# Performance work log

Hardware: AMD Instinct MI355X
Metric: run time of the kernel (lower is better)

The kernel has to match this reference:

```python
import jax, jax.numpy as jnp
import numpy as np

ALPHA = 16
M_FACTORS = [8, 16, 8]
N_FACTORS = [8, 16, 8]


def setup_inputs() -> dict:
    key = jax.random.key(0)
    ks = jax.random.split(key, 9)
    B, S, D = 8, 2048, 1024
    r = 8
    x = jax.random.normal(ks[0], (B, S, D), dtype=jnp.float32)
    W = jax.random.normal(ks[1], (D, D), dtype=jnp.float32) * 0.02
    b = jax.random.normal(ks[2], (D,), dtype=jnp.float32) * 0.02
    # m-cores: (r_prev, m_i, r_next), first rank = 1
    core0 = jax.random.normal(ks[3], (1, 8, r), dtype=jnp.float32) * 0.1
    core1 = jax.random.normal(ks[4], (r, 16, r), dtype=jnp.float32) * 0.1
    core2 = jax.random.normal(ks[5], (r, 8, r), dtype=jnp.float32) * 0.1
    # n-cores: (r_prev, n_i, r_next), last rank = 1
    core3 = jax.random.normal(ks[6], (r, 8, r), dtype=jnp.float32) * 0.1
    core4 = jax.random.normal(ks[7], (r, 16, r), dtype=jnp.float32) * 0.1
    core5 = jax.random.normal(ks[8], (r, 8, 1), dtype=jnp.float32) * 0.1
    return {"x": x, "W": W, "b": b, "core0": core0, "core1": core1,
            "core2": core2, "core3": core3, "core4": core4, "core5": core5}


def tensorized_multiplication(x, m_cores, n_cores, m_factors):
    B, S, _ = x.shape
    # [B, 1, S, m_k, ..., m_1] : input dim split into m_factors, reversed
    tt = x.reshape((B, S) + tuple(m_factors[::-1]))[:, None]
    for core in m_cores:
        # contract trailing m-factor and current rank, new rank at axis 1
        tt = jnp.einsum('br...m,rmp->bp...', tt, core)
    for core in n_cores:
        # expand n-factor at the end, carry rank at axis 1
        tt = jnp.einsum('br...,rnp->bp...n', tt, core)
    # tt: [B, 1, S, n_1, ..., n_k] -> [B, S, prod(n_factors)]
    return tt.reshape(B, S, -1)


def reference(x, W, b, core0, core1, core2, core3, core4, core5):
    z = tensorized_multiplication(x, [core0, core1, core2],
                                  [core3, core4, core5], M_FACTORS)
    base = jnp.einsum('bsd,od->bso', x, W) + b  # nn.Linear: x @ W.T + b
    return base + z * ALPHA
```

## Files before the change

### kernel.cpp

```cpp
#include <hip/hip_runtime.h>
#include <hip/hip_bf16.h>


#define D_DIM 1024
#define BS_ROWS 16384
#define ALPHA_F 16.0f
#define BM 128
#define BN 128

using bf16   = __bf16;
using bf16x8 = __attribute__((ext_vector_type(8))) __bf16;
using bf16x4 = __attribute__((ext_vector_type(4))) __bf16;
using f32x4  = __attribute__((ext_vector_type(4))) float;

#define GPTR(p) (const __attribute__((address_space(1))) void*)(p)
#define SPTR(p) (__attribute__((address_space(3))) void*)(p)

__global__ __launch_bounds__(256) void prep_kernel(
    const float* __restrict__ X,
    const float* __restrict__ W,
    const float* __restrict__ c0, const float* __restrict__ c1,
    const float* __restrict__ c2, const float* __restrict__ c3,
    const float* __restrict__ c4, const float* __restrict__ c5,
    bf16* __restrict__ Weff, bf16* __restrict__ Xb)
{
    __shared__ float t2[1024];
    __shared__ float Msh[8192];
    const int tid = threadIdx.x;

    if (blockIdx.x >= 1024) {
        size_t i = ((size_t)(blockIdx.x - 1024) * 256 + tid) * 8;
        f32x4 a = *(const f32x4*)&X[i];
        f32x4 b = *(const f32x4*)&X[i + 4];
        bf16x8 v;
        v[0] = (bf16)a[0]; v[1] = (bf16)a[1]; v[2] = (bf16)a[2]; v[3] = (bf16)a[3];
        v[4] = (bf16)b[0]; v[5] = (bf16)b[1]; v[6] = (bf16)b[2]; v[7] = (bf16)b[3];
        *(bf16x8*)&Xb[i] = v;
        return;
    }

    const int o = blockIdx.x;
    for (int e = tid; e < 1024; e += 256) {
        int p2 = e & 7, i2i1 = e >> 3;
        int i1 = i2i1 & 7, i2 = i2i1 >> 3;
        float s = 0.f;
        for (int p1 = 0; p1 < 8; ++p1)
            s += c0[i1 * 8 + p1] * c1[p1 * 128 + i2 * 8 + p2];
        t2[e] = s;
    }
    __syncthreads();
    for (int e = tid; e < 8192; e += 256) {
        int p3 = e & 7, d = e >> 3;
        int i1 = d & 7, i2 = (d >> 3) & 15, i3 = d >> 7;
        float s = 0.f;
        for (int p2 = 0; p2 < 8; ++p2)
            s += t2[(i2 * 8 + i1) * 8 + p2] * c2[p2 * 64 + i3 * 8 + p3];
        Msh[e] = s;
    }

    int n1 = o >> 7, nn = o & 127, n2 = nn >> 3, n3 = nn & 7;
    float v[8];
    for (int p4 = 0; p4 < 8; ++p4) {
        float s = 0.f;
        for (int p5 = 0; p5 < 8; ++p5)
            s += c4[p4 * 128 + n2 * 8 + p5] * c5[p5 * 8 + n3];
        v[p4] = s;
    }
    float ncol[8];
    for (int r3 = 0; r3 < 8; ++r3) {
        float s = 0.f;
        for (int p4 = 0; p4 < 8; ++p4)
            s += c3[r3 * 64 + n1 * 8 + p4] * v[p4];
        ncol[r3] = s;
    }
    __syncthreads();

    int d0 = tid * 4;
    f32x4 w = *(const f32x4*)&W[o * D_DIM + d0];
    bf16x4 res;
    for (int k = 0; k < 4; ++k) {
        float acc = 0.f;
        for (int r = 0; r < 8; ++r)
            acc += Msh[(d0 + k) * 8 + r] * ncol[r];
        res[k] = (bf16)(w[k] + ALPHA_F * acc);
    }
    *(bf16x4*)&Weff[o * D_DIM + d0] = res;
}

#define TBM 256
#define TBN 128
#define ABYTES (TBM * 128)
#define BBYTES (TBN * 128)
#define BUFB   (ABYTES + BBYTES)
#define NBUFS  3
#define NTILES (D_DIM / 64)

__global__ __launch_bounds__(512, 2) void gemm_pipe_kernel(
    const bf16* __restrict__ Xb,
    const bf16* __restrict__ Weff,
    const float* __restrict__ bias,
    float* __restrict__ Out)
{
    extern __shared__ __attribute__((aligned(16))) char smem[];

    const int tid  = threadIdx.x;
    const int wave = tid >> 6, lane = tid & 63;

    const int bid   = blockIdx.x;
    const int slot  = (bid & 7) * 64 + (bid >> 3);
    const int mtile = slot >> 3;
    const int ntile = slot & 7;

    const int wr = wave >> 1, wc = wave & 1;
    const int l15 = lane & 15, quad = lane >> 4;
    const int rsw = l15 & 7;

    const int srow   = wave * 8 + (lane >> 3);
    const int gchunk = (lane & 7) ^ (lane >> 3);
    const bf16* asrc = Xb   + (size_t)(mtile * TBM + srow) * D_DIM + gchunk * 8;
    const bf16* bsrc = Weff + (size_t)(ntile * TBN + srow) * D_DIM + gchunk * 8;
    const int woff = wave * 1024;

    auto STAGE = [&](int bo, int t) {
        const bf16* ap = asrc + t * 64;
        const bf16* bp = bsrc + t * 64;
        char* ad = smem + bo + woff;
        char* bd = smem + bo + ABYTES + woff;
#pragma unroll
        for (int j = 0; j < 4; ++j)
            __builtin_amdgcn_global_load_lds(GPTR(ap + (size_t)j * 64 * D_DIM),
                                             SPTR(ad + j * 8192), 16, 0, 0);
#pragma unroll
        for (int j = 0; j < 2; ++j)
            __builtin_amdgcn_global_load_lds(GPTR(bp + (size_t)j * 64 * D_DIM),
                                             SPTR(bd + j * 8192), 16, 0, 0);
    };

    f32x4 acc[4][4];
#pragma unroll
    for (int i = 0; i < 4; ++i)
#pragma unroll
        for (int j = 0; j < 4; ++j)
#pragma unroll
            for (int r = 0; r < 4; ++r) acc[i][j][r] = 0.f;

    auto COMPUTE = [&](int bo) {
        const bf16* Ab = (const bf16*)(smem + bo);
        const bf16* Bb = (const bf16*)(smem + bo + ABYTES);
#pragma unroll
        for (int kk = 0; kk < 2; ++kk) {
            const int sc = ((kk * 4 + quad) ^ rsw) * 8;
            bf16x8 af[4], bfr[4];
#pragma unroll
            for (int i = 0; i < 4; ++i)
                af[i] = *(const bf16x8*)&Ab[(wr * 64 + i * 16 + l15) * 64 + sc];
#pragma unroll
            for (int j = 0; j < 4; ++j)
                bfr[j] = *(const bf16x8*)&Bb[(wc * 64 + j * 16 + l15) * 64 + sc];
            __builtin_amdgcn_s_setprio(1);
#pragma unroll
            for (int i = 0; i < 4; ++i)
#pragma unroll
                for (int j = 0; j < 4; ++j)
                    acc[i][j] = __builtin_amdgcn_mfma_f32_16x16x32_bf16(
                        af[i], bfr[j], acc[i][j], 0, 0, 0);
            __builtin_amdgcn_s_setprio(0);
        }
    };

    STAGE(0, 0);
    STAGE(BUFB, 1);
    asm volatile("s_waitcnt vmcnt(6)" ::: "memory");
    __builtin_amdgcn_s_barrier();
    __builtin_amdgcn_sched_barrier(0);

    int bo = 0;
#pragma unroll
    for (int t = 0; t < NTILES - 2; ++t) {
        int bs = bo + 2 * BUFB; if (bs >= NBUFS * BUFB) bs -= NBUFS * BUFB;
        STAGE(bs, t + 2);
        COMPUTE(bo);
        asm volatile("s_waitcnt vmcnt(6) lgkmcnt(0)" ::: "memory");
        __builtin_amdgcn_s_barrier();
        __builtin_amdgcn_sched_barrier(0);
        bo += BUFB; if (bo == NBUFS * BUFB) bo = 0;
    }
    COMPUTE(bo);
    asm volatile("s_waitcnt vmcnt(0) lgkmcnt(0)" ::: "memory");
    __builtin_amdgcn_s_barrier();
    __builtin_amdgcn_sched_barrier(0);
    bo += BUFB; if (bo == NBUFS * BUFB) bo = 0;
    COMPUTE(bo);

    float bj[4];
#pragma unroll
    for (int j = 0; j < 4; ++j)
        bj[j] = bias[ntile * TBN + wc * 64 + j * 16 + l15];
#pragma unroll
    for (int i = 0; i < 4; ++i) {
        int row0 = mtile * TBM + wr * 64 + i * 16 + quad * 4;
#pragma unroll
        for (int r = 0; r < 4; ++r) {
            float* orow = Out + (size_t)(row0 + r) * D_DIM + ntile * TBN + wc * 64 + l15;
#pragma unroll
            for (int j = 0; j < 4; ++j)
                orow[j * 16] = acc[i][j][r] + bj[j];
        }
    }
}

__global__ __launch_bounds__(256) void gemm_bb_kernel(
    const bf16* __restrict__ Xb,
    const bf16* __restrict__ Weff,
    const float* __restrict__ bias,
    float* __restrict__ Out)
{
    __shared__ __align__(16) bf16 As[BM][64];
    __shared__ __align__(16) bf16 Bs[BN][64];

    const int tid  = threadIdx.x;
    const int wave = tid >> 6, lane = tid & 63;
    const int mtile = blockIdx.x, ntile = blockIdx.y;
    const int wr = wave >> 1, wc = wave & 1;
    const int l15 = lane & 15, quad = lane >> 4;

    const int srow = wave * 32 + (lane >> 3);
    const int gchunk = (lane & 7) ^ (lane >> 3);
    const bf16* asrc = Xb   + (size_t)(mtile * BM + srow) * D_DIM + gchunk * 8;
    const bf16* bsrc = Weff + (size_t)(ntile * BN + srow) * D_DIM + gchunk * 8;
    char* abase = (char*)&As[0][0] + wave * 4096;
    char* bbase = (char*)&Bs[0][0] + wave * 4096;

    const int rsw = l15 & 7;

    f32x4 acc[4][4];
    for (int i = 0; i < 4; ++i)
        for (int j = 0; j < 4; ++j)
            for (int r = 0; r < 4; ++r) acc[i][j][r] = 0.f;

    for (int kt = 0; kt < D_DIM / 64; ++kt) {
        const int ko = kt * 64;
        for (int j = 0; j < 4; ++j) {
            __builtin_amdgcn_global_load_lds(GPTR(asrc + (size_t)j * 8 * D_DIM + ko),
                                             SPTR(abase + j * 1024), 16, 0, 0);
            __builtin_amdgcn_global_load_lds(GPTR(bsrc + (size_t)j * 8 * D_DIM + ko),
                                             SPTR(bbase + j * 1024), 16, 0, 0);
        }

        __syncthreads();

        for (int kk = 0; kk < 2; ++kk) {
            const int lc = kk * 4 + quad;
            const int sc = (lc ^ rsw) * 8;
            bf16x8 af[4], bfr[4];
            for (int i = 0; i < 4; ++i)
                af[i] = *(const bf16x8*)&As[wr * 64 + i * 16 + l15][sc];
            for (int j = 0; j < 4; ++j)
                bfr[j] = *(const bf16x8*)&Bs[wc * 64 + j * 16 + l15][sc];
            for (int i = 0; i < 4; ++i)
                for (int j = 0; j < 4; ++j)
                    acc[i][j] = __builtin_amdgcn_mfma_f32_16x16x32_bf16(
                        af[i], bfr[j], acc[i][j], 0, 0, 0);
        }

        __syncthreads();
    }

    float bj[4];
    for (int j = 0; j < 4; ++j)
        bj[j] = bias[ntile * BN + wc * 64 + j * 16 + l15];
    for (int i = 0; i < 4; ++i) {
        int row0 = mtile * BM + wr * 64 + i * 16 + quad * 4;
        for (int r = 0; r < 4; ++r) {
            float* orow = Out + (size_t)(row0 + r) * D_DIM + ntile * BN + wc * 64 + l15;
            for (int j = 0; j < 4; ++j)
                orow[j * 16] = acc[i][j][r] + bj[j];
        }
    }
}

__global__ __launch_bounds__(256) void gemm_bias_kernel(
    const float* __restrict__ X,
    const bf16* __restrict__ Weff,
    const float* __restrict__ bias,
    float* __restrict__ Out)
{
    __shared__ __align__(16) bf16 As[BM][32];
    __shared__ __align__(16) bf16 Bs[BN][32];

    const int tid  = threadIdx.x;
    const int wave = tid >> 6, lane = tid & 63;
    const int mtile = blockIdx.x, ntile = blockIdx.y;
    const int wr = wave >> 1, wc = wave & 1;
    const int l15 = lane & 15, quad = lane >> 4;

    const int ar = tid >> 1, ah = tid & 1;
    const float* xsrc = X + (size_t)(mtile * BM + ar) * D_DIM + ah * 16;
    bf16* adst = &As[ar][ah * 16];

    const bf16* bsrc0 = Weff + (size_t)(ntile * BN + wave * 32 + (lane >> 2)) * D_DIM
                        + (lane & 3) * 8;
    const bf16* bsrc1 = bsrc0 + 16 * D_DIM;
    char* bbase = (char*)&Bs[0][0];
    void* bdst0 = bbase + wave * 2048;
    void* bdst1 = bbase + wave * 2048 + 1024;

    f32x4 acc[4][4];
    for (int i = 0; i < 4; ++i)
        for (int j = 0; j < 4; ++j)
            for (int r = 0; r < 4; ++r) acc[i][j][r] = 0.f;

    for (int kt = 0; kt < D_DIM / 32; ++kt) {
        __builtin_amdgcn_global_load_lds(GPTR(bsrc0 + kt * 32), SPTR(bdst0), 16, 0, 0);
        __builtin_amdgcn_global_load_lds(GPTR(bsrc1 + kt * 32), SPTR(bdst1), 16, 0, 0);

        const f32x4* xp = (const f32x4*)(xsrc + kt * 32);
        f32x4 f0 = xp[0], f1 = xp[1], f2 = xp[2], f3 = xp[3];
        bf16x8 p0, p1;
        p0[0] = (bf16)f0[0]; p0[1] = (bf16)f0[1]; p0[2] = (bf16)f0[2]; p0[3] = (bf16)f0[3];
        p0[4] = (bf16)f1[0]; p0[5] = (bf16)f1[1]; p0[6] = (bf16)f1[2]; p0[7] = (bf16)f1[3];
        p1[0] = (bf16)f2[0]; p1[1] = (bf16)f2[1]; p1[2] = (bf16)f2[2]; p1[3] = (bf16)f2[3];
        p1[4] = (bf16)f3[0]; p1[5] = (bf16)f3[1]; p1[6] = (bf16)f3[2]; p1[7] = (bf16)f3[3];
        *(bf16x8*)adst = p0;
        *(bf16x8*)(adst + 8) = p1;

        __syncthreads();

        bf16x8 af[4], bfr[4];
        for (int i = 0; i < 4; ++i)
            af[i] = *(const bf16x8*)&As[wr * 64 + i * 16 + l15][quad * 8];
        for (int j = 0; j < 4; ++j)
            bfr[j] = *(const bf16x8*)&Bs[wc * 64 + j * 16 + l15][quad * 8];
        for (int i = 0; i < 4; ++i)
            for (int j = 0; j < 4; ++j)
                acc[i][j] = __builtin_amdgcn_mfma_f32_16x16x32_bf16(
                    af[i], bfr[j], acc[i][j], 0, 0, 0);

        __syncthreads();
    }

    float bj[4];
    for (int j = 0; j < 4; ++j)
        bj[j] = bias[ntile * BN + wc * 64 + j * 16 + l15];
    for (int i = 0; i < 4; ++i) {
        int row0 = mtile * BM + wr * 64 + i * 16 + quad * 4;
        for (int r = 0; r < 4; ++r) {
            float* orow = Out + (size_t)(row0 + r) * D_DIM + ntile * BN + wc * 64 + l15;
            for (int j = 0; j < 4; ++j)
                orow[j * 16] = acc[i][j][r] + bj[j];
        }
    }
}

__global__ __launch_bounds__(256) void build_weff_fused_kernel(
    const float* __restrict__ W,
    const float* __restrict__ c0, const float* __restrict__ c1,
    const float* __restrict__ c2, const float* __restrict__ c3,
    const float* __restrict__ c4, const float* __restrict__ c5,
    bf16* __restrict__ Weff)
{
    __shared__ float t2[1024];
    __shared__ float Msh[8192];
    const int tid = threadIdx.x;
    const int o = blockIdx.x;

    for (int e = tid; e < 1024; e += 256) {
        int p2 = e & 7, i2i1 = e >> 3;
        int i1 = i2i1 & 7, i2 = i2i1 >> 3;
        float s = 0.f;
        for (int p1 = 0; p1 < 8; ++p1)
            s += c0[i1 * 8 + p1] * c1[p1 * 128 + i2 * 8 + p2];
        t2[e] = s;
    }
    __syncthreads();
    for (int e = tid; e < 8192; e += 256) {
        int p3 = e & 7, d = e >> 3;
        int i1 = d & 7, i2 = (d >> 3) & 15, i3 = d >> 7;
        float s = 0.f;
        for (int p2 = 0; p2 < 8; ++p2)
            s += t2[(i2 * 8 + i1) * 8 + p2] * c2[p2 * 64 + i3 * 8 + p3];
        Msh[e] = s;
    }
    int n1 = o >> 7, nn = o & 127, n2 = nn >> 3, n3 = nn & 7;
    float v[8];
    for (int p4 = 0; p4 < 8; ++p4) {
        float s = 0.f;
        for (int p5 = 0; p5 < 8; ++p5)
            s += c4[p4 * 128 + n2 * 8 + p5] * c5[p5 * 8 + n3];
        v[p4] = s;
    }
    float ncol[8];
    for (int r3 = 0; r3 < 8; ++r3) {
        float s = 0.f;
        for (int p4 = 0; p4 < 8; ++p4)
            s += c3[r3 * 64 + n1 * 8 + p4] * v[p4];
        ncol[r3] = s;
    }
    __syncthreads();

    int d0 = tid * 4;
    f32x4 w = *(const f32x4*)&W[o * D_DIM + d0];
    bf16x4 res;
    for (int k = 0; k < 4; ++k) {
        float acc = 0.f;
        for (int r = 0; r < 8; ++r)
            acc += Msh[(d0 + k) * 8 + r] * ncol[r];
        res[k] = (bf16)(w[k] + ALPHA_F * acc);
    }
    *(bf16x4*)&Weff[o * D_DIM + d0] = res;
}

extern "C" void kernel_launch(void* const* d_in, const int* in_sizes, int n_in,
                              void* d_out, int out_size, void* d_ws, size_t ws_size,
                              hipStream_t stream) {
    const float* x  = (const float*)d_in[0];
    const float* W  = (const float*)d_in[1];
    const float* b  = (const float*)d_in[2];
    const float* c0 = (const float*)d_in[3];
    const float* c1 = (const float*)d_in[4];
    const float* c2 = (const float*)d_in[5];
    const float* c3 = (const float*)d_in[6];
    const float* c4 = (const float*)d_in[7];
    const float* c5 = (const float*)d_in[8];
    float* out = (float*)d_out;

    char* ws = (char*)d_ws;
    bf16* Weff = (bf16*)ws;
    bf16* Xb   = (bf16*)(ws + 4u * 1024u * 1024u);
    const size_t need = 4u * 1024u * 1024u + (size_t)BS_ROWS * D_DIM * 2u;

    static int smem_ok = -1;
    if (smem_ok < 0) {
        hipError_t e = hipFuncSetAttribute((const void*)gemm_pipe_kernel,
                                           hipFuncAttributeMaxDynamicSharedMemorySize,
                                           NBUFS * BUFB);
        smem_ok = (e == hipSuccess) ? 1 : 0;
    }

    if (ws_size >= need) {
        prep_kernel<<<1024 + 8192, 256, 0, stream>>>(x, W, c0, c1, c2, c3, c4, c5,
                                                     Weff, Xb);
        if (smem_ok) {
            gemm_pipe_kernel<<<dim3(512), 512, NBUFS * BUFB, stream>>>(Xb, Weff, b, out);
        } else {
            dim3 grid(BS_ROWS / BM, D_DIM / BN);
            gemm_bb_kernel<<<grid, 256, 0, stream>>>(Xb, Weff, b, out);
        }
    } else {
        build_weff_fused_kernel<<<D_DIM, 256, 0, stream>>>(W, c0, c1, c2, c3, c4, c5, Weff);
        dim3 grid(BS_ROWS / BM, D_DIM / BN);
        gemm_bias_kernel<<<grid, 256, 0, stream>>>(x, Weff, b, out);
    }
}
```

Before: 175.3 us.

## Split TT factor prep and retile GEMM to 256x256 with 32x32 MFMA

Moves computation of the TT core products M and N^T into a single small kernel that writes them to workspace, instead of recomputing M in every one of 1024 blocks. Weff construction is then a simple elementwise-style kernel. The main GEMM is retiled to 256x256 block tiles with K=32 stages, a 4-deep LDS ring and 32x32x16 MFMA instructions, which raises arithmetic intensity per load. The risks are an extra kernel launch, a grid of only 256 blocks for the GEMM, and higher register pressure from the 32x32 accumulators.

```diff
diff --git a/kernel.cpp b/kernel.cpp
--- a/kernel.cpp
+++ b/kernel.cpp
@@ -12,24 +12,65 @@
 using bf16x8 = __attribute__((ext_vector_type(8))) __bf16;
 using bf16x4 = __attribute__((ext_vector_type(4))) __bf16;
 using f32x4  = __attribute__((ext_vector_type(4))) float;
+using f32x16 = __attribute__((ext_vector_type(16))) float;
 
 #define GPTR(p) (const __attribute__((address_space(1))) void*)(p)
 #define SPTR(p) (__attribute__((address_space(3))) void*)(p)
 
-__global__ __launch_bounds__(256) void prep_kernel(
-    const float* __restrict__ X,
-    const float* __restrict__ W,
+__global__ __launch_bounds__(256) void make_mn_kernel(
     const float* __restrict__ c0, const float* __restrict__ c1,
     const float* __restrict__ c2, const float* __restrict__ c3,
     const float* __restrict__ c4, const float* __restrict__ c5,
+    float* __restrict__ Mws, float* __restrict__ NTws)
+{
+    __shared__ float t2[128 * 9];
+    __shared__ float vt[128 * 9];
+    const int tid = threadIdx.x;
+
+    for (int e = tid; e < 1024; e += 256) {
+        int p2 = e & 7, i2i1 = e >> 3;
+        int i1 = i2i1 & 7, i2 = i2i1 >> 3;
+        float s = 0.f;
+        for (int p1 = 0; p1 < 8; ++p1)
+            s += c0[i1 * 8 + p1] * c1[p1 * 128 + i2 * 8 + p2];
+        t2[i2i1 * 9 + p2] = s;
+    }
+    __syncthreads();
+    for (int e = tid; e < 8192; e += 256) {
+        int p3 = e & 7, d = e >> 3;
+        int i1 = d & 7, i2 = (d >> 3) & 15, i3 = d >> 7;
+        float s = 0.f;
+        for (int p2 = 0; p2 < 8; ++p2)
+            s += t2[(i2 * 8 + i1) * 9 + p2] * c2[p2 * 64 + i3 * 8 + p3];
+        Mws[e] = s;
+    }
+    for (int e = tid; e < 1024; e += 256) {
+        int p4 = e & 7, nn = e >> 3;
+        int n2 = nn >> 3, n3 = nn & 7;
+        float s = 0.f;
+        for (int p5 = 0; p5 < 8; ++p5)
+            s += c4[p4 * 128 + n2 * 8 + p5] * c5[p5 * 8 + n3];
+        vt[nn * 9 + p4] = s;
+    }
+    __syncthreads();
+    for (int e = tid; e < 8192; e += 256) {
+        int r3 = e & 7, o = e >> 3;
+        int n1 = o >> 7, nn = o & 127;
+        float s = 0.f;
+        for (int p4 = 0; p4 < 8; ++p4)
+            s += c3[r3 * 64 + n1 * 8 + p4] * vt[nn * 9 + p4];
+        NTws[o * 8 + r3] = s;
+    }
+}
+
+__global__ __launch_bounds__(256) void weff_cast_kernel(
+    const float* __restrict__ X, const float* __restrict__ W,
+    const float* __restrict__ Mws, const float* __restrict__ NTws,
     bf16* __restrict__ Weff, bf16* __restrict__ Xb)
 {
-    __shared__ float t2[1024];
-    __shared__ float Msh[8192];
     const int tid = threadIdx.x;
-
-    if (blockIdx.x >= 1024) {
-        size_t i = ((size_t)(blockIdx.x - 1024) * 256 + tid) * 8;
+    if (blockIdx.x >= 512) {
+        size_t i = ((size_t)(blockIdx.x - 512) * 256 + tid) * 8;
         f32x4 a = *(const f32x4*)&X[i];
         f32x4 b = *(const f32x4*)&X[i + 4];
         bf16x8 v;
@@ -38,64 +79,35 @@
         *(bf16x8*)&Xb[i] = v;
         return;
     }
-
-    const int o = blockIdx.x;
-    for (int e = tid; e < 1024; e += 256) {
-        int p2 = e & 7, i2i1 = e >> 3;
-        int i1 = i2i1 & 7, i2 = i2i1 >> 3;
-        float s = 0.f;
-        for (int p1 = 0; p1 < 8; ++p1)
-            s += c0[i1 * 8 + p1] * c1[p1 * 128 + i2 * 8 + p2];
-        t2[e] = s;
-    }
-    __syncthreads();
-    for (int e = tid; e < 8192; e += 256) {
-        int p3 = e & 7, d = e >> 3;
-        int i1 = d & 7, i2 = (d >> 3) & 15, i3 = d >> 7;
-        float s = 0.f;
-        for (int p2 = 0; p2 < 8; ++p2)
-            s += t2[(i2 * 8 + i1) * 8 + p2] * c2[p2 * 64 + i3 * 8 + p3];
-        Msh[e] = s;
-    }
-
-    int n1 = o >> 7, nn = o & 127, n2 = nn >> 3, n3 = nn & 7;
-    float v[8];
-    for (int p4 = 0; p4 < 8; ++p4) {
-        float s = 0.f;
-        for (int p5 = 0; p5 < 8; ++p5)
-            s += c4[p4 * 128 + n2 * 8 + p5] * c5[p5 * 8 + n3];
-        v[p4] = s;
-    }
-    float ncol[8];
-    for (int r3 = 0; r3 < 8; ++r3) {
-        float s = 0.f;
-        for (int p4 = 0; p4 < 8; ++p4)
-            s += c3[r3 * 64 + n1 * 8 + p4] * v[p4];
-        ncol[r3] = s;
-    }
-    __syncthreads();
-
-    int d0 = tid * 4;
-    f32x4 w = *(const f32x4*)&W[o * D_DIM + d0];
-    bf16x4 res;
-    for (int k = 0; k < 4; ++k) {
-        float acc = 0.f;
-        for (int r = 0; r < 8; ++r)
-            acc += Msh[(d0 + k) * 8 + r] * ncol[r];
-        res[k] = (bf16)(w[k] + ALPHA_F * acc);
-    }
-    *(bf16x4*)&Weff[o * D_DIM + d0] = res;
+    int e  = blockIdx.x * 256 + tid;
+    int o  = e >> 7;
+    int d0 = (e & 127) * 8;
+    f32x4 nt0 = *(const f32x4*)&NTws[o * 8];
+    f32x4 nt1 = *(const f32x4*)&NTws[o * 8 + 4];
+    f32x4 w0 = *(const f32x4*)&W[(size_t)o * D_DIM + d0];
+    f32x4 w1 = *(const f32x4*)&W[(size_t)o * D_DIM + d0 + 4];
+    bf16x8 res;
+    for (int k = 0; k < 8; ++k) {
+        f32x4 m0 = *(const f32x4*)&Mws[(d0 + k) * 8];
+        f32x4 m1 = *(const f32x4*)&Mws[(d0 + k) * 8 + 4];
+        float acc = m0[0]*nt0[0] + m0[1]*nt0[1] + m0[2]*nt0[2] + m0[3]*nt0[3]
+                  + m1[0]*nt1[0] + m1[1]*nt1[1] + m1[2]*nt1[2] + m1[3]*nt1[3];
+        float w = (k < 4) ? w0[k] : w1[k - 4];
+        res[k] = (bf16)(w + ALPHA_F * acc);
+    }
+    *(bf16x8*)&Weff[(size_t)o * D_DIM + d0] = res;
 }
 
 #define TBM 256
-#define TBN 128
-#define ABYTES (TBM * 128)
-#define BBYTES (TBN * 128)
-#define BUFB   (ABYTES + BBYTES)
-#define NBUFS  3
-#define NTILES (D_DIM / 64)
-
-__global__ __launch_bounds__(512, 2) void gemm_pipe_kernel(
+#define TBN 256
+#define TBK 32
+#define ABYT (TBM * TBK * 2)
+#define BBYT (TBN * TBK * 2)
+#define BUF2 (ABYT + BBYT)
+#define NB2  4
+#define NT2  (D_DIM / TBK)
+
+__global__ __launch_bounds__(512, 2) void gemm_pipe2_kernel(
     const bf16* __restrict__ Xb,
     const bf16* __restrict__ Weff,
     const float* __restrict__ bias,
@@ -107,104 +119,109 @@
     const int wave = tid >> 6, lane = tid & 63;
 
     const int bid   = blockIdx.x;
-    const int slot  = (bid & 7) * 64 + (bid >> 3);
-    const int mtile = slot >> 3;
-    const int ntile = slot & 7;
-
-    const int wr = wave >> 1, wc = wave & 1;
-    const int l15 = lane & 15, quad = lane >> 4;
-    const int rsw = l15 & 7;
-
-    const int srow   = wave * 8 + (lane >> 3);
-    const int gchunk = (lane & 7) ^ (lane >> 3);
-    const bf16* asrc = Xb   + (size_t)(mtile * TBM + srow) * D_DIM + gchunk * 8;
-    const bf16* bsrc = Weff + (size_t)(ntile * TBN + srow) * D_DIM + gchunk * 8;
+    const int slot  = (bid & 7) * 32 + (bid >> 3);
+    const int mtile = slot >> 2;
+    const int ntile = slot & 3;
+
+    const int wr = wave >> 2, wc = wave & 3;
+    const int l31 = lane & 31, half = lane >> 5;
+    const int swz = (l31 >> 1) & 3;
+
+    const int srow   = wave * 16 + (lane >> 2);
+    const int lchunk = (lane & 3) ^ ((lane >> 3) & 3);
+    const bf16* asrc = Xb   + (size_t)(mtile * TBM + srow) * D_DIM + lchunk * 8;
+    const bf16* bsrc = Weff + (size_t)(ntile * TBN + srow) * D_DIM + lchunk * 8;
     const int woff = wave * 1024;
 
     auto STAGE = [&](int bo, int t) {
-        const bf16* ap = asrc + t * 64;
-        const bf16* bp = bsrc + t * 64;
-        char* ad = smem + bo + woff;
-        char* bd = smem + bo + ABYTES + woff;
-#pragma unroll
-        for (int j = 0; j < 4; ++j)
-            __builtin_amdgcn_global_load_lds(GPTR(ap + (size_t)j * 64 * D_DIM),
-                                             SPTR(ad + j * 8192), 16, 0, 0);
+        const bf16* ap = asrc + t * TBK;
+        const bf16* bp = bsrc + t * TBK;
+        __builtin_amdgcn_global_load_lds(GPTR(ap),
+                                         SPTR(smem + bo + woff), 16, 0, 0);
+        __builtin_amdgcn_global_load_lds(GPTR(ap + (size_t)128 * D_DIM),
+                                         SPTR(smem + bo + 8192 + woff), 16, 0, 0);
+        __builtin_amdgcn_global_load_lds(GPTR(bp),
+                                         SPTR(smem + bo + ABYT + woff), 16, 0, 0);
+        __builtin_amdgcn_global_load_lds(GPTR(bp + (size_t)128 * D_DIM),
+                                         SPTR(smem + bo + ABYT + 8192 + woff), 16, 0, 0);
+    };
+
+    f32x16 acc[4][2];
+#pragma unroll
+    for (int i = 0; i < 4; ++i)
 #pragma unroll
         for (int j = 0; j < 2; ++j)
-            __builtin_amdgcn_global_load_lds(GPTR(bp + (size_t)j * 64 * D_DIM),
-                                             SPTR(bd + j * 8192), 16, 0, 0);
-    };
-
-    f32x4 acc[4][4];
-#pragma unroll
-    for (int i = 0; i < 4; ++i)
-#pragma unroll
-        for (int j = 0; j < 4; ++j)
-#pragma unroll
-            for (int r = 0; r < 4; ++r) acc[i][j][r] = 0.f;
+#pragma unroll
+            for (int r = 0; r < 16; ++r) acc[i][j][r] = 0.f;
 
     auto COMPUTE = [&](int bo) {
-        const bf16* Ab = (const bf16*)(smem + bo);
-        const bf16* Bb = (const bf16*)(smem + bo + ABYTES);
+        const char* Ab = smem + bo;
+        const char* Bb = smem + bo + ABYT;
 #pragma unroll
         for (int kk = 0; kk < 2; ++kk) {
-            const int sc = ((kk * 4 + quad) ^ rsw) * 8;
-            bf16x8 af[4], bfr[4];
+            const int sc16 = (((kk * 2 + half) ^ swz) * 16);
+            bf16x8 af[4], bfr[2];
 #pragma unroll
             for (int i = 0; i < 4; ++i)
-                af[i] = *(const bf16x8*)&Ab[(wr * 64 + i * 16 + l15) * 64 + sc];
-#pragma unroll
-            for (int j = 0; j < 4; ++j)
-                bfr[j] = *(const bf16x8*)&Bb[(wc * 64 + j * 16 + l15) * 64 + sc];
+                af[i] = *(const bf16x8*)(Ab + (wr * 128 + i * 32 + l31) * 64 + sc16);
+#pragma unroll
+            for (int j = 0; j < 2; ++j)
+                bfr[j] = *(const bf16x8*)(Bb + (wc * 64 + j * 32 + l31) * 64 + sc16);
             __builtin_amdgcn_s_setprio(1);
 #pragma unroll
             for (int i = 0; i < 4; ++i)
 #pragma unroll
-                for (int j = 0; j < 4; ++j)
-                    acc[i][j] = __builtin_amdgcn_mfma_f32_16x16x32_bf16(
+                for (int j = 0; j < 2; ++j)
+                    acc[i][j] = __builtin_amdgcn_mfma_f32_32x32x16_bf16(
                         af[i], bfr[j], acc[i][j], 0, 0, 0);
             __builtin_amdgcn_s_setprio(0);
         }
     };
 
     STAGE(0, 0);
-    STAGE(BUFB, 1);
-    asm volatile("s_waitcnt vmcnt(6)" ::: "memory");
+    STAGE(BUF2, 1);
+    STAGE(2 * BUF2, 2);
+    asm volatile("s_waitcnt vmcnt(8)" ::: "memory");
     __builtin_amdgcn_s_barrier();
     __builtin_amdgcn_sched_barrier(0);
 
     int bo = 0;
-#pragma unroll
-    for (int t = 0; t < NTILES - 2; ++t) {
-        int bs = bo + 2 * BUFB; if (bs >= NBUFS * BUFB) bs -= NBUFS * BUFB;
-        STAGE(bs, t + 2);
+    for (int t = 0; t < NT2 - 3; ++t) {
+        int bs = bo + 3 * BUF2; if (bs >= NB2 * BUF2) bs -= NB2 * BUF2;
+        STAGE(bs, t + 3);
         COMPUTE(bo);
-        asm volatile("s_waitcnt vmcnt(6) lgkmcnt(0)" ::: "memory");
+        asm volatile("s_waitcnt vmcnt(8) lgkmcnt(0)" ::: "memory");
         __builtin_amdgcn_s_barrier();
         __builtin_amdgcn_sched_barrier(0);
-        bo += BUFB; if (bo == NBUFS * BUFB) bo = 0;
-    }
+        bo += BUF2; if (bo == NB2 * BUF2) bo = 0;
+    }
+    COMPUTE(bo);
+    asm volatile("s_waitcnt vmcnt(4) lgkmcnt(0)" ::: "memory");
+    __builtin_amdgcn_s_barrier();
+    __builtin_amdgcn_sched_barrier(0);
+    bo += BUF2; if (bo == NB2 * BUF2) bo = 0;
     COMPUTE(bo);
     asm volatile("s_waitcnt vmcnt(0) lgkmcnt(0)" ::: "memory");
     __builtin_amdgcn_s_barrier();
     __builtin_amdgcn_sched_barrier(0);
-    bo += BUFB; if (bo == NBUFS * BUFB) bo = 0;
+    bo += BUF2; if (bo == NB2 * BUF2) bo = 0;
     COMPUTE(bo);
 
-    float bj[4];
-#pragma unroll
-    for (int j = 0; j < 4; ++j)
-        bj[j] = bias[ntile * TBN + wc * 64 + j * 16 + l15];
+    float bj[2];
+#pragma unroll
+    for (int j = 0; j < 2; ++j)
+        bj[j] = bias[ntile * TBN + wc * 64 + j * 32 + l31];
 #pragma unroll
     for (int i = 0; i < 4; ++i) {
-        int row0 = mtile * TBM + wr * 64 + i * 16 + quad * 4;
-#pragma unroll
-        for (int r = 0; r < 4; ++r) {
-            float* orow = Out + (size_t)(row0 + r) * D_DIM + ntile * TBN + wc * 64 + l15;
-#pragma unroll
-            for (int j = 0; j < 4; ++j)
-                orow[j * 16] = acc[i][j][r] + bj[j];
+        int rbase = mtile * TBM + wr * 128 + i * 32 + 4 * half;
+#pragma unroll
+        for (int j = 0; j < 2; ++j) {
+            int col = ntile * TBN + wc * 64 + j * 32 + l31;
+#pragma unroll
+            for (int r = 0; r < 16; ++r) {
+                int row = rbase + (r & 3) + 8 * (r >> 2);
+                Out[(size_t)row * D_DIM + col] = acc[i][j][r] + bj[j];
+            }
         }
     }
 }
@@ -246,9 +263,7 @@
             __builtin_amdgcn_global_load_lds(GPTR(bsrc + (size_t)j * 8 * D_DIM + ko),
                                              SPTR(bbase + j * 1024), 16, 0, 0);
         }
-
         __syncthreads();
-
         for (int kk = 0; kk < 2; ++kk) {
             const int lc = kk * 4 + quad;
             const int sc = (lc ^ rsw) * 8;
@@ -262,7 +277,6 @@
                     acc[i][j] = __builtin_amdgcn_mfma_f32_16x16x32_bf16(
                         af[i], bfr[j], acc[i][j], 0, 0, 0);
         }
-
         __syncthreads();
     }
 
@@ -425,23 +439,25 @@
     float* out = (float*)d_out;
 
     char* ws = (char*)d_ws;
-    bf16* Weff = (bf16*)ws;
-    bf16* Xb   = (bf16*)(ws + 4u * 1024u * 1024u);
+    bf16*  Weff = (bf16*)ws;
+    float* Mws  = (float*)(ws + 2u * 1024u * 1024u);
+    float* NTws = Mws + 8192;
+    bf16*  Xb   = (bf16*)(ws + 4u * 1024u * 1024u);
     const size_t need = 4u * 1024u * 1024u + (size_t)BS_ROWS * D_DIM * 2u;
 
     static int smem_ok = -1;
     if (smem_ok < 0) {
-        hipError_t e = hipFuncSetAttribute((const void*)gemm_pipe_kernel,
+        hipError_t e = hipFuncSetAttribute((const void*)gemm_pipe2_kernel,
                                            hipFuncAttributeMaxDynamicSharedMemorySize,
-                                           NBUFS * BUFB);
+                                           NB2 * BUF2);
         smem_ok = (e == hipSuccess) ? 1 : 0;
     }
 
     if (ws_size >= need) {
-        prep_kernel<<<1024 + 8192, 256, 0, stream>>>(x, W, c0, c1, c2, c3, c4, c5,
-                                                     Weff, Xb);
+        make_mn_kernel<<<1, 256, 0, stream>>>(c0, c1, c2, c3, c4, c5, Mws, NTws);
+        weff_cast_kernel<<<512 + 8192, 256, 0, stream>>>(x, W, Mws, NTws, Weff, Xb);
         if (smem_ok) {
-            gemm_pipe_kernel<<<dim3(512), 512, NBUFS * BUFB, stream>>>(Xb, Weff, b, out);
+            gemm_pipe2_kernel<<<dim3(256), 512, NB2 * BUF2, stream>>>(Xb, Weff, b, out);
         } else {
             dim3 grid(BS_ROWS / BM, D_DIM / BN);
             gemm_bb_kernel<<<grid, 256, 0, stream>>>(Xb, Weff, b, out);
```

Result: slower. 184.6 us (+5.3%).
